# Optimization experiments

Hardware: AMD Instinct MI355X
Metric: run time of the kernel (lower is better)

The kernel has to match this reference:

```python
import jax, jax.numpy as jnp
import numpy as np

TOKEN_SIZE = 16
STRIDE = 8
EMBED_DIM = 512


def setup_inputs() -> dict:
    key = jax.random.key(0)
    k1, k2 = jax.random.split(key)
    B, S, D = 32, 4096, EMBED_DIM
    x = jax.random.normal(k1, (B, S, D), dtype=jnp.float32)
    fan_in = TOKEN_SIZE * D
    W = jax.random.normal(k2, (fan_in, D), dtype=jnp.float32) / np.sqrt(fan_in)
    b = jnp.zeros((D,), dtype=jnp.float32)
    gamma = jnp.ones((D,), dtype=jnp.float32)
    beta = jnp.zeros((D,), dtype=jnp.float32)
    return {"x": x, "W": W, "b": b, "gamma": gamma, "beta": beta}


def reference(x, W, b, gamma, beta):
    B, S, D = x.shape
    n_win = (S - TOKEN_SIZE) // STRIDE + 1
    # gather all sliding windows at once: [n_win, token_size] index matrix
    idx = jnp.arange(n_win)[:, None] * STRIDE + jnp.arange(TOKEN_SIZE)[None, :]
    win = x[:, idx, :]                       # [B, n_win, token_size, D]
    win = win.reshape(B, n_win, TOKEN_SIZE * D)  # flatten each window
    h = jnp.einsum('bnf,fd->bnd', win, W) + b    # batched GEMM
    h = jax.nn.gelu(h, approximate=False)        # torch GELU default = exact erf
    # LayerNorm over last dim (eps matches torch default 1e-5)
    mu = jnp.mean(h, axis=-1, keepdims=True)
    var = jnp.var(h, axis=-1, keepdims=True)
    h = (h - mu) * jax.lax.rsqrt(var + 1e-5)
    return h * gamma + beta                      # [B, n_win, D]
```

## Files before the change

### kernel.cpp

```cpp
#include <hip/hip_runtime.h>
#include <hip/hip_bf16.h>
#include <cstdint>

#define S_LEN 4096
#define D_DIM 512
#define NWIN  511
#define KDIM  8192
#define TROWS 520
#define ASLOTS (TROWS * 8)

typedef __attribute__((ext_vector_type(8))) short short8;
typedef __attribute__((ext_vector_type(4))) float f32x4;

__device__ __forceinline__ unsigned short f2b(float f) {
    union { float f; unsigned int u; } v; v.f = f;
    unsigned int r = v.u + 0x7FFFu + ((v.u >> 16) & 1u);
    return (unsigned short)(r >> 16);
}

__global__ void wpack_kernel(const float* __restrict__ W, short8* __restrict__ pk) {
    __shared__ float tile[64][68];
    const int b2 = blockIdx.x;
    const int s = b2 >> 3, w = b2 & 7;
    const int t = s >> 3, c0 = (s & 7) << 6;
    const int tid = threadIdx.x;
    {
        int r = tid >> 2, c4 = (tid & 3) << 4;
        const float* src = W + (size_t)(t * 512 + c0 + r) * D_DIM + (w << 6) + c4;
#pragma unroll
        for (int j = 0; j < 4; ++j) {
            float4 v = *(const float4*)(src + 4 * j);
            tile[r][c4 + 4 * j + 0] = v.x;
            tile[r][c4 + 4 * j + 1] = v.y;
            tile[r][c4 + 4 * j + 2] = v.z;
            tile[r][c4 + 4 * j + 3] = v.w;
        }
    }
    __syncthreads();
    const int lane = tid & 63, f2 = tid >> 6;
#pragma unroll
    for (int ff = 0; ff < 2; ++ff) {
        int f = f2 * 2 + ff;
        int n = f >> 1, k32 = f & 1;
        short8 u;
#pragma unroll
        for (int e = 0; e < 8; ++e)
            u[e] = (short)f2b(tile[k32 * 32 + (lane >> 4) * 8 + e][n * 16 + (lane & 15)]);
        pk[((size_t)b2 * 8 + f) * 64 + lane] = u;
    }
}

__device__ __forceinline__ void load_b(const short8* __restrict__ pk, int s, int wslot,
                                       int lane, short8 (&b)[4][2]) {
    const short8* base = pk + ((size_t)(s * 8 + wslot) * 8) * 64 + lane;
#pragma unroll
    for (int n = 0; n < 4; ++n)
#pragma unroll
        for (int k32 = 0; k32 < 2; ++k32)
            b[n][k32] = base[(n * 2 + k32) * 64];
}

__device__ __forceinline__ void stage_a(const float* __restrict__ xb, int n0, int tid,
                                        int c0, unsigned short* __restrict__ lsA) {
#pragma unroll 4
    for (int it = 0; it < 17; ++it) {
        int slot = tid + (it << 8);
        if (slot < ASLOTS) {
            int r = slot >> 3, k8 = slot & 7;
            int grow = 8 * n0 + r;
            if (grow > S_LEN - 1) grow = S_LEN - 1;
            const float* src = xb + (size_t)grow * D_DIM + (c0 << 6) + (k8 << 3);
            float4 a0 = *(const float4*)src;
            float4 a1 = *(const float4*)(src + 4);
            short8 u;
            u[0] = (short)f2b(a0.x); u[1] = (short)f2b(a0.y);
            u[2] = (short)f2b(a0.z); u[3] = (short)f2b(a0.w);
            u[4] = (short)f2b(a1.x); u[5] = (short)f2b(a1.y);
            u[6] = (short)f2b(a1.z); u[7] = (short)f2b(a1.w);
            *(short8*)&lsA[(r << 6) + ((k8 ^ ((r >> 3) & 7)) << 3)] = u;
        }
    }
}

__global__ __launch_bounds__(256, 2)
void gemm_kernel(const float* __restrict__ x,
                 const short8* __restrict__ pk,
                 const float* __restrict__ bias,
                 float* __restrict__ hout)
{
    __shared__ __align__(16) unsigned short lsA[TROWS * 64];

    const int p  = blockIdx.x;
    const int g  = ((p >> 4) << 3) | (p & 7);
    const int nc = (p >> 3) & 1;
    const int b  = g >> 3;
    const int n0 = (g & 7) << 6;
    const int tid  = threadIdx.x;
    const int lane = tid & 63, wid = tid >> 6;
    const int wslot = nc * 4 + wid;
    const int r15 = lane & 15, hi = lane >> 4;
    const float* xb = x + (size_t)b * S_LEN * D_DIM;

    f32x4 acc[4][4] = {};
    short8 bc[4][2], bn[4][2];

    load_b(pk, 0, wslot, lane, bc);
    stage_a(xb, n0, tid, 0, lsA);
    asm volatile("s_waitcnt lgkmcnt(0)" ::: "memory");
    __builtin_amdgcn_s_barrier();
    __builtin_amdgcn_sched_barrier(0);

#define TSTEP(T, BCUR, BNXT)                                                   \
    {                                                                          \
        const int sn = ((T) < 15) ? (((T) + 1) * 8 + c0) : ((c0 + 1) & 7);     \
        load_b(pk, sn, wslot, lane, BNXT);                                     \
        short8 afr[4][2];                                                      \
        _Pragma("unroll")                                                      \
        for (int m = 0; m < 4; ++m) {                                          \
            int row = (((m << 4) + r15) << 3) + (T);                           \
            int sb  = (r15 + ((T) >> 3)) & 7;                                  \
            _Pragma("unroll")                                                  \
            for (int k32 = 0; k32 < 2; ++k32) {                                \
                int swz = ((k32 << 2) + hi) ^ sb;                              \
                afr[m][k32] = *(const short8*)&lsA[(row << 6) + (swz << 3)];   \
            }                                                                  \
        }                                                                      \
        _Pragma("unroll")                                                      \
        for (int k32 = 0; k32 < 2; ++k32)                                      \
            _Pragma("unroll")                                                  \
            for (int m = 0; m < 4; ++m)                                        \
                _Pragma("unroll")                                              \
                for (int n = 0; n < 4; ++n)                                    \
                    acc[m][n] = __builtin_amdgcn_mfma_f32_16x16x32_bf16(       \
                        afr[m][k32], BCUR[n][k32], acc[m][n], 0, 0, 0);        \
    }

    for (int c0 = 0; c0 < 8; ++c0) {
#pragma unroll
        for (int tt = 0; tt < 8; ++tt) {
            TSTEP(2 * tt,     bc, bn)
            TSTEP(2 * tt + 1, bn, bc)
        }
        __builtin_amdgcn_s_barrier();
        __builtin_amdgcn_sched_barrier(0);
        if (c0 < 7) {
            stage_a(xb, n0, tid, c0 + 1, lsA);
            asm volatile("s_waitcnt lgkmcnt(0)" ::: "memory");
            __builtin_amdgcn_s_barrier();
            __builtin_amdgcn_sched_barrier(0);
        }
    }
#undef TSTEP

    float bias4[4];
#pragma unroll
    for (int n = 0; n < 4; ++n)
        bias4[n] = bias[(wslot << 6) + (n << 4) + r15];
    float* hb = hout + (size_t)b * NWIN * D_DIM;
#pragma unroll
    for (int m = 0; m < 4; ++m) {
#pragma unroll
        for (int r = 0; r < 4; ++r) {
            int win = n0 + (m << 4) + (hi << 2) + r;
            if (win < NWIN) {
                size_t obase = (size_t)win * D_DIM + (wslot << 6) + r15;
#pragma unroll
                for (int n = 0; n < 4; ++n) {
                    float h = acc[m][n][r] + bias4[n];
                    float gl = 0.5f * h * (1.0f + erff(h * 0.70710678118654752f));
                    hb[obase + (n << 4)] = gl;
                }
            }
        }
    }
}

__global__ __launch_bounds__(256, 8)
void ln_kernel(const float* __restrict__ h, const float* __restrict__ gamma,
               const float* __restrict__ beta, float* __restrict__ out, int nrows)
{
    const int lane = threadIdx.x & 63;
    const int wv = blockIdx.x * 4 + (threadIdx.x >> 6);
    const int nw = gridDim.x * 4;
    float gm[8], bt[8];
#pragma unroll
    for (int j = 0; j < 8; ++j) {
        gm[j] = gamma[lane * 8 + j];
        bt[j] = beta[lane * 8 + j];
    }
    for (int row = wv; row < nrows; row += nw) {
        const float* src = h + (size_t)row * D_DIM + lane * 8;
        float4 v0 = *(const float4*)src;
        float4 v1 = *(const float4*)(src + 4);
        float s = v0.x + v0.y + v0.z + v0.w + v1.x + v1.y + v1.z + v1.w;
        float q = v0.x * v0.x + v0.y * v0.y + v0.z * v0.z + v0.w * v0.w +
                  v1.x * v1.x + v1.y * v1.y + v1.z * v1.z + v1.w * v1.w;
#pragma unroll
        for (int msk = 1; msk < 64; msk <<= 1) {
            s += __shfl_xor(s, msk, 64);
            q += __shfl_xor(q, msk, 64);
        }
        float mu  = s * (1.0f / 512.0f);
        float inv = rsqrtf(q * (1.0f / 512.0f) - mu * mu + 1e-5f);
        float o[8] = { v0.x, v0.y, v0.z, v0.w, v1.x, v1.y, v1.z, v1.w };
        float4 r0, r1;
        r0.x = (o[0] - mu) * inv * gm[0] + bt[0];
        r0.y = (o[1] - mu) * inv * gm[1] + bt[1];
        r0.z = (o[2] - mu) * inv * gm[2] + bt[2];
        r0.w = (o[3] - mu) * inv * gm[3] + bt[3];
        r1.x = (o[4] - mu) * inv * gm[4] + bt[4];
        r1.y = (o[5] - mu) * inv * gm[5] + bt[5];
        r1.z = (o[6] - mu) * inv * gm[6] + bt[6];
        r1.w = (o[7] - mu) * inv * gm[7] + bt[7];
        float* dst = out + (size_t)row * D_DIM + lane * 8;
        *(float4*)dst = r0;
        *(float4*)(dst + 4) = r1;
    }
}

__global__ __launch_bounds__(512, 2)
void fused_kernel(const float* __restrict__ x,
                  const short8* __restrict__ pk,
                  const float* __restrict__ bias,
                  const float* __restrict__ gamma,
                  const float* __restrict__ beta,
                  float* __restrict__ out)
{
    __shared__ __align__(16) unsigned short lsA[2][64 * 64];
    __shared__ float redS[8][64];
    __shared__ float redQ[8][64];

    const int blk = blockIdx.x;
    const int b  = blk >> 3;
    const int n0 = (blk & 7) << 6;
    const int tid = threadIdx.x;
    const int lane = tid & 63;
    const int wid  = tid >> 6;
    const int r15 = lane & 15, hi = lane >> 4;
    const int ai = tid >> 3, ak8 = tid & 7;
    const int akb = ak8 ^ (ai & 7);
    const float* xb = x + (size_t)b * S_LEN * D_DIM;

    f32x4 acc[4][4] = {};
    short8 bc[4][2], bn[4][2];
    {
        int row = 8 * (n0 + ai) + 0;
        if (row > S_LEN - 1) row = S_LEN - 1;
        const float* src = xb + (size_t)row * D_DIM + 0 + ak8 * 8;
        float4 f0 = *(const float4*)src;
        float4 f1 = *(const float4*)(src + 4);
        short8 u;
        u[0] = (short)f2b(f0.x); u[1] = (short)f2b(f0.y);
        u[2] = (short)f2b(f0.z); u[3] = (short)f2b(f0.w);
        u[4] = (short)f2b(f1.x); u[5] = (short)f2b(f1.y);
        u[6] = (short)f2b(f1.z); u[7] = (short)f2b(f1.w);
        *(short8*)&lsA[0][ai * 64 + akb * 8] = u;
        load_b(pk, 0, wid, lane, bc);
    }
    __syncthreads();

#define STEP(S, CUR, NXT, BCUR, BNXT)                                          \
    {                                                                          \
        const int sn = ((S) + 1) & 127;                                        \
        const int tn = sn >> 3, c0n = (sn & 7) << 6;                           \
        int rown = 8 * (n0 + ai) + tn;                                         \
        if (rown > S_LEN - 1) rown = S_LEN - 1;                                \
        const float* asrc = xb + (size_t)rown * D_DIM + c0n + ak8 * 8;         \
        float4 f0 = *(const float4*)asrc;                                      \
        float4 f1 = *(const float4*)(asrc + 4);                                \
        load_b(pk, sn, wid, lane, BNXT);                                       \
        short8 afr[4][2];                                                      \
        _Pragma("unroll")                                                      \
        for (int m = 0; m < 4; ++m) {                                          \
            int row = 16 * m + r15;                                            \
            _Pragma("unroll")                                                  \
            for (int k32 = 0; k32 < 2; ++k32) {                                \
                int kb = (k32 * 4 + hi) ^ (row & 7);                           \
                afr[m][k32] = *(const short8*)&lsA[CUR][row * 64 + kb * 8];    \
            }                                                                  \
        }                                                                      \
        _Pragma("unroll")                                                      \
        for (int k32 = 0; k32 < 2; ++k32)                                      \
            _Pragma("unroll")                                                  \
            for (int m = 0; m < 4; ++m)                                        \
                _Pragma("unroll")                                              \
                for (int n = 0; n < 4; ++n)                                    \
                    acc[m][n] = __builtin_amdgcn_mfma_f32_16x16x32_bf16(       \
                        afr[m][k32], BCUR[n][k32], acc[m][n], 0, 0, 0);        \
        short8 u;                                                              \
        u[0] = (short)f2b(f0.x); u[1] = (short)f2b(f0.y);                      \
        u[2] = (short)f2b(f0.z); u[3] = (short)f2b(f0.w);                      \
        u[4] = (short)f2b(f1.x); u[5] = (short)f2b(f1.y);                      \
        u[6] = (short)f2b(f1.z); u[7] = (short)f2b(f1.w);                      \
        *(short8*)&lsA[NXT][ai * 64 + akb * 8] = u;                            \
        asm volatile("s_waitcnt lgkmcnt(0)" ::: "memory");                     \
        __builtin_amdgcn_s_barrier();                                          \
        __builtin_amdgcn_sched_barrier(0);                                     \
    }

    for (int it = 0; it < 64; ++it) {
        STEP(it * 2,     0, 1, bc, bn)
        STEP(it * 2 + 1, 1, 0, bn, bc)
    }
#undef STEP

    float bias4[4], gam4[4], bet4[4];
#pragma unroll
    for (int n = 0; n < 4; ++n) {
        int d = (wid << 6) + 16 * n + r15;
        bias4[n] = bias[d]; gam4[n] = gamma[d]; bet4[n] = beta[d];
    }
    float sum_[4][4], sq_[4][4];
#pragma unroll
    for (int m = 0; m < 4; ++m)
#pragma unroll
        for (int r = 0; r < 4; ++r) { sum_[m][r] = 0.f; sq_[m][r] = 0.f; }
#pragma unroll
    for (int m = 0; m < 4; ++m)
#pragma unroll
        for (int n = 0; n < 4; ++n)
#pragma unroll
            for (int r = 0; r < 4; ++r) {
                float h = acc[m][n][r] + bias4[n];
                float g = 0.5f * h * (1.0f + erff(h * 0.70710678118654752f));
                acc[m][n][r] = g;
                sum_[m][r] += g;
                sq_[m][r]  += g * g;
            }
#pragma unroll
    for (int m = 0; m < 4; ++m)
#pragma unroll
        for (int r = 0; r < 4; ++r) {
            float sv = sum_[m][r], qv = sq_[m][r];
#pragma unroll
            for (int msk = 1; msk < 16; msk <<= 1) {
                sv += __shfl_xor(sv, msk, 64);
                qv += __shfl_xor(qv, msk, 64);
            }
            sum_[m][r] = sv; sq_[m][r] = qv;
        }
    if (r15 == 0) {
#pragma unroll
        for (int m = 0; m < 4; ++m)
#pragma unroll
            for (int r = 0; r < 4; ++r) {
                int row16 = 16 * m + hi * 4 + r;
                redS[wid][row16] = sum_[m][r];
                redQ[wid][row16] = sq_[m][r];
            }
    }
    __syncthreads();
#pragma unroll
    for (int m = 0; m < 4; ++m) {
#pragma unroll
        for (int r = 0; r < 4; ++r) {
            int row16 = 16 * m + hi * 4 + r;
            float sv = 0.f, qv = 0.f;
#pragma unroll
            for (int w = 0; w < 8; ++w) { sv += redS[w][row16]; qv += redQ[w][row16]; }
            float mu  = sv * (1.0f / 512.0f);
            float var = qv * (1.0f / 512.0f) - mu * mu;
            float inv = rsqrtf(var + 1e-5f);
            int win = n0 + row16;
            if (win < NWIN) {
                size_t obase = ((size_t)b * NWIN + win) * D_DIM;
#pragma unroll
                for (int n = 0; n < 4; ++n) {
                    int d = (wid << 6) + 16 * n + r15;
                    out[obase + d] = (acc[m][n][r] - mu) * inv * gam4[n] + bet4[n];
                }
            }
        }
    }
}

__global__ void naive_kernel(const float* __restrict__ x, const float* __restrict__ W,
                             const float* __restrict__ bias, const float* __restrict__ gamma,
                             const float* __restrict__ beta, float* __restrict__ out) {
    __shared__ float hrow[D_DIM];
    __shared__ float red[2];
    const int b = blockIdx.x / NWIN, win = blockIdx.x % NWIN;
    const int d = threadIdx.x;
    float a = 0.f;
    for (int t = 0; t < 16; ++t) {
        const float* xr = x + ((size_t)b * S_LEN + 8 * win + t) * D_DIM;
        const float* wr = W + (size_t)t * D_DIM * D_DIM;
        for (int k = 0; k < D_DIM; ++k) a += xr[k] * wr[(size_t)k * D_DIM + d];
    }
    a += bias[d];
    a = 0.5f * a * (1.0f + erff(a * 0.70710678118654752f));
    hrow[d] = a;
    __syncthreads();
    if (d == 0) {
        float s = 0.f, q = 0.f;
        for (int k = 0; k < D_DIM; ++k) { s += hrow[k]; q += hrow[k] * hrow[k]; }
        float mu = s / D_DIM;
        red[0] = mu; red[1] = rsqrtf(q / D_DIM - mu * mu + 1e-5f);
    }
    __syncthreads();
    out[((size_t)b * NWIN + win) * D_DIM + d] = (a - red[0]) * red[1] * gamma[d] + beta[d];
}

extern "C" void kernel_launch(void* const* d_in, const int* in_sizes, int n_in,
                              void* d_out, int out_size, void* d_ws, size_t ws_size,
                              hipStream_t stream) {
    const float* x     = (const float*)d_in[0];
    const float* W     = (const float*)d_in[1];
    const float* bias  = (const float*)d_in[2];
    const float* gamma = (const float*)d_in[3];
    const float* beta  = (const float*)d_in[4];
    float* out = (float*)d_out;

    const size_t pk_bytes = (size_t)KDIM * D_DIM * sizeof(unsigned short);
    const size_t h_bytes  = (size_t)32 * NWIN * D_DIM * sizeof(float);

    if (ws_size >= pk_bytes + h_bytes) {
        short8* pk = (short8*)d_ws;
        float* hbuf = (float*)((char*)d_ws + pk_bytes);
        wpack_kernel<<<1024, 256, 0, stream>>>(W, pk);
        gemm_kernel<<<512, 256, 0, stream>>>(x, pk, bias, hbuf);
        ln_kernel<<<1024, 256, 0, stream>>>(hbuf, gamma, beta, out, 32 * NWIN);
    } else if (ws_size >= pk_bytes) {
        short8* pk = (short8*)d_ws;
        wpack_kernel<<<1024, 256, 0, stream>>>(W, pk);
        fused_kernel<<<256, 512, 0, stream>>>(x, pk, bias, gamma, beta, out);
    } else {
        naive_kernel<<<32 * NWIN, D_DIM, 0, stream>>>(x, W, bias, gamma, beta, out);
    }
}
```

Before: 208.2 us.

## Double M-tile per block and prefetch next A chunk during MFMA steps

The GEMM block grows to 512 threads covering 128 windows, so each staged A chunk in LDS is reused by twice as many waves and the grid halves to 256 blocks. Global loads and bf16 conversion of the next A chunk are interleaved between MFMA steps into registers, then written to LDS after a barrier, rather than staged serially. The aim is to hide x-load latency behind compute and cut redundant A staging. The cost is much higher register pressure (17 short8 staging registers plus temporaries) at one block per CU, which risks spills or lower occupancy.

New measurement: 254.3 us. 22.1% more time.

```diff
diff --git a/kernel.cpp b/kernel.cpp
--- a/kernel.cpp
+++ b/kernel.cpp
@@ -6,7 +6,8 @@
 #define D_DIM 512
 #define NWIN  511
 #define KDIM  8192
-#define TROWS 520
+#define BMW   128
+#define TROWS (8 * BMW + 8)
 #define ASLOTS (TROWS * 8)
 
 typedef __attribute__((ext_vector_type(8))) short short8;
@@ -60,29 +61,55 @@
             b[n][k32] = base[(n * 2 + k32) * 64];
 }
 
-__device__ __forceinline__ void stage_a(const float* __restrict__ xb, int n0, int tid,
-                                        int c0, unsigned short* __restrict__ lsA) {
-#pragma unroll 4
+__device__ __forceinline__ void a_issue(const float* __restrict__ xb, int n0, int tid,
+                                        int c0n, int i0, int cnt, float4 (&t)[3][2]) {
+#pragma unroll
+    for (int j = 0; j < 3; ++j) {
+        if (j < cnt) {
+            int slot = tid + (i0 + j) * 512;
+            if (slot < ASLOTS) {
+                int r = slot >> 3, k8 = slot & 7;
+                int grow = 8 * n0 + r;
+                if (grow > S_LEN - 1) grow = S_LEN - 1;
+                const float* src = xb + (size_t)grow * D_DIM + (c0n << 6) + (k8 << 3);
+                t[j][0] = *(const float4*)src;
+                t[j][1] = *(const float4*)(src + 4);
+            }
+        }
+    }
+}
+
+__device__ __forceinline__ void a_cvt(int tid, int i0, int cnt,
+                                      const float4 (&t)[3][2], short8 (&su)[17]) {
+#pragma unroll
+    for (int j = 0; j < 3; ++j) {
+        if (j < cnt) {
+            int slot = tid + (i0 + j) * 512;
+            if (slot < ASLOTS) {
+                short8 u;
+                u[0] = (short)f2b(t[j][0].x); u[1] = (short)f2b(t[j][0].y);
+                u[2] = (short)f2b(t[j][0].z); u[3] = (short)f2b(t[j][0].w);
+                u[4] = (short)f2b(t[j][1].x); u[5] = (short)f2b(t[j][1].y);
+                u[6] = (short)f2b(t[j][1].z); u[7] = (short)f2b(t[j][1].w);
+                su[i0 + j] = u;
+            }
+        }
+    }
+}
+
+__device__ __forceinline__ void a_write(unsigned short* __restrict__ lsA, int tid,
+                                        const short8 (&su)[17]) {
+#pragma unroll
     for (int it = 0; it < 17; ++it) {
-        int slot = tid + (it << 8);
+        int slot = tid + it * 512;
         if (slot < ASLOTS) {
             int r = slot >> 3, k8 = slot & 7;
-            int grow = 8 * n0 + r;
-            if (grow > S_LEN - 1) grow = S_LEN - 1;
-            const float* src = xb + (size_t)grow * D_DIM + (c0 << 6) + (k8 << 3);
-            float4 a0 = *(const float4*)src;
-            float4 a1 = *(const float4*)(src + 4);
-            short8 u;
-            u[0] = (short)f2b(a0.x); u[1] = (short)f2b(a0.y);
-            u[2] = (short)f2b(a0.z); u[3] = (short)f2b(a0.w);
-            u[4] = (short)f2b(a1.x); u[5] = (short)f2b(a1.y);
-            u[6] = (short)f2b(a1.z); u[7] = (short)f2b(a1.w);
-            *(short8*)&lsA[(r << 6) + ((k8 ^ ((r >> 3) & 7)) << 3)] = u;
-        }
-    }
-}
-
-__global__ __launch_bounds__(256, 2)
+            *(short8*)&lsA[(r << 6) + ((k8 ^ ((r >> 3) & 7)) << 3)] = su[it];
+        }
+    }
+}
+
+__global__ __launch_bounds__(512, 1)
 void gemm_kernel(const float* __restrict__ x,
                  const short8* __restrict__ pk,
                  const float* __restrict__ bias,
@@ -91,21 +118,36 @@
     __shared__ __align__(16) unsigned short lsA[TROWS * 64];
 
     const int p  = blockIdx.x;
-    const int g  = ((p >> 4) << 3) | (p & 7);
-    const int nc = (p >> 3) & 1;
-    const int b  = g >> 3;
-    const int n0 = (g & 7) << 6;
+    const int nc = (p & 7) >> 2;
+    const int g  = ((p >> 3) << 2) | (p & 3);
+    const int b  = g >> 2;
+    const int n0 = (g & 3) << 7;
     const int tid  = threadIdx.x;
     const int lane = tid & 63, wid = tid >> 6;
-    const int wslot = nc * 4 + wid;
+    const int wr = wid >> 2, wc = wid & 3;
+    const int wslot = nc * 4 + wc;
     const int r15 = lane & 15, hi = lane >> 4;
     const float* xb = x + (size_t)b * S_LEN * D_DIM;
 
     f32x4 acc[4][4] = {};
     short8 bc[4][2], bn[4][2];
+    short8 su[17];
+    float4 tmp0[3][2], tmp1[3][2];
 
     load_b(pk, 0, wslot, lane, bc);
-    stage_a(xb, n0, tid, 0, lsA);
+
+    a_issue(xb, n0, tid, 0, 0, 3, tmp0);
+#pragma unroll
+    for (int k = 0; k < 6; ++k) {
+        int cnt = (k < 5) ? 3 : 2;
+        if (k < 5) {
+            if (k & 1) a_issue(xb, n0, tid, 0, 3 * (k + 1), (k + 1 < 5) ? 3 : 2, tmp0);
+            else       a_issue(xb, n0, tid, 0, 3 * (k + 1), (k + 1 < 5) ? 3 : 2, tmp1);
+        }
+        if (k & 1) a_cvt(tid, 3 * k, cnt, tmp1, su);
+        else       a_cvt(tid, 3 * k, cnt, tmp0, su);
+    }
+    a_write(lsA, tid, su);
     asm volatile("s_waitcnt lgkmcnt(0)" ::: "memory");
     __builtin_amdgcn_s_barrier();
     __builtin_amdgcn_sched_barrier(0);
@@ -117,7 +159,7 @@
         short8 afr[4][2];                                                      \
         _Pragma("unroll")                                                      \
         for (int m = 0; m < 4; ++m) {                                          \
-            int row = (((m << 4) + r15) << 3) + (T);                           \
+            int row = (((wr << 6) + (m << 4) + r15) << 3) + (T);               \
             int sb  = (r15 + ((T) >> 3)) & 7;                                  \
             _Pragma("unroll")                                                  \
             for (int k32 = 0; k32 < 2; ++k32) {                                \
@@ -136,15 +178,33 @@
     }
 
     for (int c0 = 0; c0 < 8; ++c0) {
-#pragma unroll
-        for (int tt = 0; tt < 8; ++tt) {
-            TSTEP(2 * tt,     bc, bn)
-            TSTEP(2 * tt + 1, bn, bc)
-        }
+        const int pf = (c0 < 7) ? 1 : 0;
+        TSTEP(0, bc, bn)
+        TSTEP(1, bn, bc)
+        if (pf) a_issue(xb, n0, tid, c0 + 1, 0, 3, tmp0);
+        TSTEP(2, bc, bn)
+        TSTEP(3, bn, bc)
+        if (pf) { a_cvt(tid, 0, 3, tmp0, su); a_issue(xb, n0, tid, c0 + 1, 3, 3, tmp1); }
+        TSTEP(4, bc, bn)
+        TSTEP(5, bn, bc)
+        if (pf) { a_cvt(tid, 3, 3, tmp1, su); a_issue(xb, n0, tid, c0 + 1, 6, 3, tmp0); }
+        TSTEP(6, bc, bn)
+        TSTEP(7, bn, bc)
+        if (pf) { a_cvt(tid, 6, 3, tmp0, su); a_issue(xb, n0, tid, c0 + 1, 9, 3, tmp1); }
+        TSTEP(8, bc, bn)
+        TSTEP(9, bn, bc)
+        if (pf) { a_cvt(tid, 9, 3, tmp1, su); a_issue(xb, n0, tid, c0 + 1, 12, 3, tmp0); }
+        TSTEP(10, bc, bn)
+        TSTEP(11, bn, bc)
+        if (pf) { a_cvt(tid, 12, 3, tmp0, su); a_issue(xb, n0, tid, c0 + 1, 15, 2, tmp1); }
+        TSTEP(12, bc, bn)
+        TSTEP(13, bn, bc)
+        if (pf) a_cvt(tid, 15, 2, tmp1, su);
+        TSTEP(14, bc, bn)
+        TSTEP(15, bn, bc)
         __builtin_amdgcn_s_barrier();
-        __builtin_amdgcn_sched_barrier(0);
-        if (c0 < 7) {
-            stage_a(xb, n0, tid, c0 + 1, lsA);
+        if (pf) {
+            a_write(lsA, tid, su);
             asm volatile("s_waitcnt lgkmcnt(0)" ::: "memory");
             __builtin_amdgcn_s_barrier();
             __builtin_amdgcn_sched_barrier(0);
@@ -161,7 +221,7 @@
     for (int m = 0; m < 4; ++m) {
 #pragma unroll
         for (int r = 0; r < 4; ++r) {
-            int win = n0 + (m << 4) + (hi << 2) + r;
+            int win = n0 + (wr << 6) + (m << 4) + (hi << 2) + r;
             if (win < NWIN) {
                 size_t obase = (size_t)win * D_DIM + (wslot << 6) + r15;
 #pragma unroll
@@ -226,7 +286,7 @@
                   const float* __restrict__ beta,
                   float* __restrict__ out)
 {
-    __shared__ __align__(16) unsigned short lsA[2][64 * 64];
+    __shared__ __align__(16) unsigned short lsAf[2][64 * 64];
     __shared__ float redS[8][64];
     __shared__ float redQ[8][64];
 
@@ -254,7 +314,7 @@
         u[2] = (short)f2b(f0.z); u[3] = (short)f2b(f0.w);
         u[4] = (short)f2b(f1.x); u[5] = (short)f2b(f1.y);
         u[6] = (short)f2b(f1.z); u[7] = (short)f2b(f1.w);
-        *(short8*)&lsA[0][ai * 64 + akb * 8] = u;
+        *(short8*)&lsAf[0][ai * 64 + akb * 8] = u;
         load_b(pk, 0, wid, lane, bc);
     }
     __syncthreads();
@@ -276,7 +336,7 @@
             _Pragma("unroll")                                                  \
             for (int k32 = 0; k32 < 2; ++k32) {                                \
                 int kb = (k32 * 4 + hi) ^ (row & 7);                           \
-                afr[m][k32] = *(const short8*)&lsA[CUR][row * 64 + kb * 8];    \
+                afr[m][k32] = *(const short8*)&lsAf[CUR][row * 64 + kb * 8];   \
             }                                                                  \
         }                                                                      \
         _Pragma("unroll")                                                      \
@@ -292,7 +352,7 @@
         u[2] = (short)f2b(f0.z); u[3] = (short)f2b(f0.w);                      \
         u[4] = (short)f2b(f1.x); u[5] = (short)f2b(f1.y);                      \
         u[6] = (short)f2b(f1.z); u[7] = (short)f2b(f1.w);                      \
-        *(short8*)&lsA[NXT][ai * 64 + akb * 8] = u;                            \
+        *(short8*)&lsAf[NXT][ai * 64 + akb * 8] = u;                           \
         asm volatile("s_waitcnt lgkmcnt(0)" ::: "memory");                     \
         __builtin_amdgcn_s_barrier();                                          \
         __builtin_amdgcn_sched_barrier(0);                                     \
@@ -418,7 +478,7 @@
         short8* pk = (short8*)d_ws;
         float* hbuf = (float*)((char*)d_ws + pk_bytes);
         wpack_kernel<<<1024, 256, 0, stream>>>(W, pk);
-        gemm_kernel<<<512, 256, 0, stream>>>(x, pk, bias, hbuf);
+        gemm_kernel<<<256, 512, 0, stream>>>(x, pk, bias, hbuf);
         ln_kernel<<<1024, 256, 0, stream>>>(hbuf, gamma, beta, out, 32 * NWIN);
     } else if (ws_size >= pk_bytes) {
         short8* pk = (short8*)d_ws;
```
